# Performance work log

Hardware: AMD Instinct MI355X
Metric: run time of the kernel (lower is better)

Reference implementation:

```python
import jax, jax.numpy as jnp
import numpy as np

N_NODES = 100000
N_EDGES = 3200000
N_F = 128
HIDDEN = 128
N_PRED = 8
K_HOPS = 3
N_GRAPHS = 64


def setup_inputs() -> dict:
    key = jax.random.key(0)
    k1, k2, k3, k4, k5, k6, k7, k8 = jax.random.split(key, 8)
    x = jax.random.normal(k1, (N_NODES, N_F), dtype=jnp.float32)
    edge_index = jax.random.randint(k2, (2, N_EDGES), 0, N_NODES, dtype=jnp.int64)
    edge_attr = jax.random.uniform(k3, (N_EDGES,), dtype=jnp.float32)
    batch = jnp.sort(jax.random.randint(k4, (N_NODES,), 0, N_GRAPHS, dtype=jnp.int64))
    # SGConv internal Linear: in=n_f, out=hidden (applied after K propagations)
    s1 = 1.0 / np.sqrt(N_F)
    W_conv = jax.random.uniform(k5, (HIDDEN, N_F), dtype=jnp.float32, minval=-s1, maxval=s1)
    b_conv = jax.random.uniform(k6, (HIDDEN,), dtype=jnp.float32, minval=-s1, maxval=s1)
    s2 = 1.0 / np.sqrt(HIDDEN)
    W_lin = jax.random.uniform(k7, (N_PRED, HIDDEN), dtype=jnp.float32, minval=-s2, maxval=s2)
    b_lin = jax.random.uniform(k8, (N_PRED,), dtype=jnp.float32, minval=-s2, maxval=s2)
    return {"x": x, "edge_index": edge_index, "edge_attr": edge_attr, "batch": batch,
            "W_conv": W_conv, "b_conv": b_conv, "W_lin": W_lin, "b_lin": b_lin}


def _gcn_norm(edge_index, edge_weight, num_nodes):
    # Add self-loops with weight 1 (PyG gcn_norm default), then symmetric normalize.
    loop = jnp.arange(num_nodes, dtype=edge_index.dtype)
    row = jnp.concatenate([edge_index[0], loop])
    col = jnp.concatenate([edge_index[1], loop])
    w = jnp.concatenate([edge_weight, jnp.ones((num_nodes,), dtype=edge_weight.dtype)])
    deg = jax.ops.segment_sum(w, col, num_segments=num_nodes)
    dinv = jnp.where(deg > 0, jax.lax.rsqrt(jnp.where(deg > 0, deg, 1.0)), 0.0)
    norm = dinv[row] * w * dinv[col]
    return row, col, norm


def reference(x, edge_index, edge_attr, batch, W_conv, b_conv, W_lin, b_lin):
    N = x.shape[0]
    row, col, norm = _gcn_norm(edge_index, edge_attr, N)
    h = x
    for _ in range(K_HOPS):  # K repeated gather-scale-scatter propagations
        h = jax.ops.segment_sum(norm[:, None] * h[row], col, num_segments=N)
    h = h @ W_conv.T + b_conv  # SGConv linear: [N, hidden]
    # global_mean_pool by batch id
    sums = jax.ops.segment_sum(h, batch, num_segments=N_GRAPHS)
    cnt = jax.ops.segment_sum(jnp.ones((N,), dtype=h.dtype), batch, num_segments=N_GRAPHS)
    pooled = sums / jnp.maximum(cnt, 1.0)[:, None]
    # dropout(p=0.5) is identity in eval mode
    return pooled @ W_lin.T + b_lin
```

## Files before the change

kernel.cpp:

```cpp
#include <hip/hip_runtime.h>

#define NN 100000
#define NE 3200000
#define NF 128
#define NH 128
#define NP 8
#define NG 64

#define CS 16000
#define NC 7
#define NW 64
#define ES (NE / NW)

#define PT 64
#define GP 1024

#define SCAN_B 1024
#define SCAN_NBLK 98

__device__ __forceinline__ unsigned short f2bf(float f) {
    unsigned u = __float_as_uint(f);
    return (unsigned short)((u + 0x7fffu + ((u >> 16) & 1u)) >> 16);
}
__device__ __forceinline__ float bf2f(unsigned short b) {
    return __uint_as_float((unsigned)b << 16);
}

__global__ void k_init(float* __restrict__ cnt, float* __restrict__ psum) {
    int i = blockIdx.x * blockDim.x + threadIdx.x;
    if (i < NG) cnt[i] = 0.0f;
    if (i < NG * NH) psum[i] = 0.0f;
}

__global__ __launch_bounds__(256) void k_hist(const int* __restrict__ row,
                                              unsigned* __restrict__ H) {
    __shared__ unsigned hist[CS];
    int w = blockIdx.x % NW, c = blockIdx.x / NW;
    int rbase = c * CS;
    int nb = (rbase + CS <= NN) ? CS : (NN - rbase);
    for (int i = threadIdx.x; i < nb; i += 256) hist[i] = 0u;
    __syncthreads();
    const int4* r4 = (const int4*)(row + (size_t)w * ES);
    for (int i = threadIdx.x; i < ES / 8; i += 256) {
        int4 a = r4[2 * i], b = r4[2 * i + 1];
        int rs[8] = {a.x, a.y, a.z, a.w, b.x, b.y, b.z, b.w};
#pragma unroll
        for (int j = 0; j < 8; ++j) {
            unsigned rr = (unsigned)(rs[j] - rbase);
            if (rr < (unsigned)nb) atomicAdd(&hist[rr], 1u);
        }
    }
    __syncthreads();
    for (int i = threadIdx.x; i < nb; i += 256) H[(size_t)w * NN + rbase + i] = hist[i];
}

__global__ __launch_bounds__(256) void k_deg_hist(const int* __restrict__ col,
                                                  const float* __restrict__ wt,
                                                  float* __restrict__ Hd) {
    __shared__ float dh[CS];
    int w = blockIdx.x % NW, c = blockIdx.x / NW;
    int rbase = c * CS;
    int nb = (rbase + CS <= NN) ? CS : (NN - rbase);
    for (int i = threadIdx.x; i < nb; i += 256) dh[i] = 0.0f;
    __syncthreads();
    const int4*   c4 = (const int4*)(col + (size_t)w * ES);
    const float4* w4 = (const float4*)(wt + (size_t)w * ES);
    for (int i = threadIdx.x; i < ES / 8; i += 256) {
        int4 a = c4[2 * i], b = c4[2 * i + 1];
        float4 wa = w4[2 * i], wb = w4[2 * i + 1];
        int cc[8] = {a.x, a.y, a.z, a.w, b.x, b.y, b.z, b.w};
        float ww[8] = {wa.x, wa.y, wa.z, wa.w, wb.x, wb.y, wb.z, wb.w};
#pragma unroll
        for (int j = 0; j < 8; ++j) {
            unsigned rr = (unsigned)(cc[j] - rbase);
            if (rr < (unsigned)nb) atomicAdd(&dh[rr], ww[j]);
        }
    }
    __syncthreads();
    for (int i = threadIdx.x; i < nb; i += 256) Hd[(size_t)w * NN + rbase + i] = dh[i];
}

__global__ void k_cnt(const int* __restrict__ batch, float* __restrict__ cnt) {
    __shared__ float c[NG];
    int t = threadIdx.x;
    if (t < NG) c[t] = 0.0f;
    __syncthreads();
    int i = blockIdx.x * blockDim.x + t;
    if (i < NN) atomicAdd(&c[batch[i]], 1.0f);
    __syncthreads();
    if (t < NG && c[t] != 0.0f) atomicAdd(&cnt[t], c[t]);
}

__global__ void k_reduce(const unsigned* __restrict__ H, const float* __restrict__ Hd,
                         int* __restrict__ rcnt, float* __restrict__ dinv) {
    int r = blockIdx.x * blockDim.x + threadIdx.x;
    if (r >= NN) return;
    unsigned s = 0;
    float d = 1.0f;
#pragma unroll
    for (int w = 0; w < NW; ++w) {
        s += H[(size_t)w * NN + r];
        d += Hd[(size_t)w * NN + r];
    }
    rcnt[r] = (int)s;
    dinv[r] = rsqrtf(d);
}

__global__ __launch_bounds__(SCAN_B) void k_scan1(const int* __restrict__ rcnt,
                                                  int* __restrict__ px,
                                                  int* __restrict__ bsum) {
    __shared__ int s[SCAN_B];
    int t = threadIdx.x;
    int i = blockIdx.x * SCAN_B + t;
    int v = (i < NN) ? rcnt[i] : 0;
    s[t] = v;
    __syncthreads();
    for (int off = 1; off < SCAN_B; off <<= 1) {
        int x = (t >= off) ? s[t - off] : 0;
        __syncthreads();
        s[t] += x;
        __syncthreads();
    }
    px[i] = s[t] - v;
    if (t == SCAN_B - 1) bsum[blockIdx.x] = s[t];
}

__global__ void k_scan2(const int* __restrict__ bsum, int* __restrict__ bofs) {
    if (threadIdx.x == 0) {
        int acc = 0;
        for (int b = 0; b < SCAN_NBLK; ++b) { bofs[b] = acc; acc += bsum[b]; }
    }
}

__global__ void k_scan3(const int* __restrict__ px, const int* __restrict__ bofs,
                        int* __restrict__ rowptr) {
    int i = blockIdx.x * blockDim.x + threadIdx.x;
    if (i > NN) return;
    rowptr[i] = px[i] + bofs[i >> 10];
}

__global__ void k_base(const int* __restrict__ rowptr, unsigned* __restrict__ H) {
    int r = blockIdx.x * blockDim.x + threadIdx.x;
    if (r >= NN) return;
    unsigned acc = (unsigned)rowptr[r];
#pragma unroll
    for (int w = 0; w < NW; ++w) {
        unsigned v = H[(size_t)w * NN + r];
        H[(size_t)w * NN + r] = acc;
        acc += v;
    }
}

__global__ __launch_bounds__(256) void k_sort(const int* __restrict__ row,
                                              const int* __restrict__ col,
                                              const float* __restrict__ wt,
                                              const unsigned* __restrict__ B,
                                              const float* __restrict__ dinv,
                                              float2* __restrict__ pack) {
    __shared__ unsigned basel[CS];
    int w = blockIdx.x % NW, c = blockIdx.x / NW;
    int rbase = c * CS;
    int nb = (rbase + CS <= NN) ? CS : (NN - rbase);
    for (int i = threadIdx.x; i < nb; i += 256)
        basel[i] = B[(size_t)w * NN + rbase + i];
    __syncthreads();
    const int4*   r4 = (const int4*)(row + (size_t)w * ES);
    const int4*   c4 = (const int4*)(col + (size_t)w * ES);
    const float4* w4 = (const float4*)(wt + (size_t)w * ES);
    for (int i = threadIdx.x; i < ES / 8; i += 256) {
        int4 ra = r4[2 * i], rb = r4[2 * i + 1];
        int4 ca = c4[2 * i], cb = c4[2 * i + 1];
        float4 wa = w4[2 * i], wb = w4[2 * i + 1];
        int rs[8] = {ra.x, ra.y, ra.z, ra.w, rb.x, rb.y, rb.z, rb.w};
        int cs[8] = {ca.x, ca.y, ca.z, ca.w, cb.x, cb.y, cb.z, cb.w};
        float ww[8] = {wa.x, wa.y, wa.z, wa.w, wb.x, wb.y, wb.z, wb.w};
#pragma unroll
        for (int j = 0; j < 8; ++j) {
            unsigned rr = (unsigned)(rs[j] - rbase);
            if (rr < (unsigned)nb) {
                unsigned pos = atomicAdd(&basel[rr], 1u);
                pack[pos] = make_float2(__int_as_float(cs[j]),
                                        dinv[rs[j]] * ww[j] * dinv[cs[j]]);
            }
        }
    }
}

__global__ void k_q1_gather(const int* __restrict__ rowptr, const float2* __restrict__ pack,
                            const int* __restrict__ batch, const float* __restrict__ dinv,
                            unsigned short* __restrict__ Q) {
    int wid = (blockIdx.x * blockDim.x + threadIdx.x) >> 6;
    int lane = threadIdx.x & 63;
    if (wid >= NN) return;
    int es = lane >> 3;
    int gg = lane & 7;
    int beg = rowptr[wid], end = rowptr[wid + 1];
    float d = dinv[wid];
    int bself = batch[wid];
    float dd = d * d;
    float acc[8];
#pragma unroll
    for (int i = 0; i < 8; ++i)
        acc[i] = (es == 0 && bself == gg * 8 + i) ? dd : 0.0f;

    if (beg < end) {
        int last = end - 1;
        int idx0 = beg + es; if (idx0 > last) idx0 = last;
        float2 pe = pack[idx0];
        for (int e = beg; e < end; e += 8) {
            int nidx = e + 8 + es; if (nidx > last) nidx = last;
            float2 pnext = pack[nidx];
            int   cc = __float_as_int(pe.x);
            float w  = (e + es <= last) ? pe.y : 0.0f;
            int b = batch[cc];
#pragma unroll
            for (int i = 0; i < 8; ++i) acc[i] += (b == gg * 8 + i) ? w : 0.0f;
            pe = pnext;
        }
    }
#pragma unroll
    for (int m = 8; m <= 32; m <<= 1)
#pragma unroll
        for (int i = 0; i < 8; ++i) acc[i] += __shfl_xor(acc[i], m, 64);
    if (es == 0) {
        uint4 o;
        o.x = (unsigned)f2bf(acc[0]) | ((unsigned)f2bf(acc[1]) << 16);
        o.y = (unsigned)f2bf(acc[2]) | ((unsigned)f2bf(acc[3]) << 16);
        o.z = (unsigned)f2bf(acc[4]) | ((unsigned)f2bf(acc[5]) << 16);
        o.w = (unsigned)f2bf(acc[6]) | ((unsigned)f2bf(acc[7]) << 16);
        ((uint4*)Q)[(size_t)wid * 8 + gg] = o;
    }
}

__global__ void k_hop_gather(const int* __restrict__ rowptr, const float2* __restrict__ pack,
                             const float* __restrict__ dinv,
                             const unsigned short* __restrict__ Qin,
                             unsigned short* __restrict__ Qout) {
    int wid = (blockIdx.x * blockDim.x + threadIdx.x) >> 6;
    int lane = threadIdx.x & 63;
    if (wid >= NN) return;
    int es = lane >> 3;
    int gg = lane & 7;
    int beg = rowptr[wid], end = rowptr[wid + 1];
    float d = dinv[wid];
    const uint4* Q4 = (const uint4*)Qin;

    float acc[8];
    if (es == 0) {
        uint4 qs = Q4[(size_t)wid * 8 + gg];
        float dd = d * d;
        acc[0] = dd * __uint_as_float(qs.x << 16);
        acc[1] = dd * __uint_as_float(qs.x & 0xffff0000u);
        acc[2] = dd * __uint_as_float(qs.y << 16);
        acc[3] = dd * __uint_as_float(qs.y & 0xffff0000u);
        acc[4] = dd * __uint_as_float(qs.z << 16);
        acc[5] = dd * __uint_as_float(qs.z & 0xffff0000u);
        acc[6] = dd * __uint_as_float(qs.w << 16);
        acc[7] = dd * __uint_as_float(qs.w & 0xffff0000u);
    } else {
#pragma unroll
        for (int i = 0; i < 8; ++i) acc[i] = 0.0f;
    }

    if (beg < end) {
        int last = end - 1;
        int idx0 = beg + es; if (idx0 > last) idx0 = last;
        float2 pe = pack[idx0];
        for (int e = beg; e < end; e += 8) {
            int nidx = e + 8 + es; if (nidx > last) nidx = last;
            float2 pnext = pack[nidx];
            int   cc = __float_as_int(pe.x);
            float w  = (e + es <= last) ? pe.y : 0.0f;
            uint4 qv = Q4[(size_t)cc * 8 + gg];
            acc[0] += w * __uint_as_float(qv.x << 16);
            acc[1] += w * __uint_as_float(qv.x & 0xffff0000u);
            acc[2] += w * __uint_as_float(qv.y << 16);
            acc[3] += w * __uint_as_float(qv.y & 0xffff0000u);
            acc[4] += w * __uint_as_float(qv.z << 16);
            acc[5] += w * __uint_as_float(qv.z & 0xffff0000u);
            acc[6] += w * __uint_as_float(qv.w << 16);
            acc[7] += w * __uint_as_float(qv.w & 0xffff0000u);
            pe = pnext;
        }
    }
#pragma unroll
    for (int m = 8; m <= 32; m <<= 1)
#pragma unroll
        for (int i = 0; i < 8; ++i) acc[i] += __shfl_xor(acc[i], m, 64);
    if (es == 0) {
        uint4 o;
        o.x = (unsigned)f2bf(acc[0]) | ((unsigned)f2bf(acc[1]) << 16);
        o.y = (unsigned)f2bf(acc[2]) | ((unsigned)f2bf(acc[3]) << 16);
        o.z = (unsigned)f2bf(acc[4]) | ((unsigned)f2bf(acc[5]) << 16);
        o.w = (unsigned)f2bf(acc[6]) | ((unsigned)f2bf(acc[7]) << 16);
        ((uint4*)Qout)[(size_t)wid * 8 + gg] = o;
    }
}

__global__ __launch_bounds__(256) void k_pool(const unsigned short* __restrict__ Q,
                                              const float* __restrict__ x,
                                              float* __restrict__ partial) {
    __shared__ unsigned short qsh[PT * NG];
    __shared__ float xs[PT * NF];
    int t = threadIdx.x;
    int f4 = (t & 31) << 2;
    int g0 = (t >> 5) << 3;
    float4 acc[8];
#pragma unroll
    for (int i = 0; i < 8; ++i) acc[i] = make_float4(0.f, 0.f, 0.f, 0.f);

    const int NT = (NN + PT - 1) / PT;
    for (int tile = blockIdx.x; tile < NT; tile += GP) {
        int n0 = tile * PT;
        int nt = min(PT, NN - n0);
        const uint4*  Q4 = (const uint4*)(Q + (size_t)n0 * NG);
        const float4* X4 = (const float4*)(x + (size_t)n0 * NF);
        uint4*  qs4 = (uint4*)qsh;
        float4* xs4 = (float4*)xs;
        for (int i = t; i < nt * (NG / 8); i += 256) qs4[i] = Q4[i];
        for (int i = t; i < nt * (NF / 4); i += 256) xs4[i] = X4[i];
        __syncthreads();
        for (int n = 0; n < nt; ++n) {
            float4 xv = *(const float4*)&xs[n * NF + f4];
            uint4 qu = *(const uint4*)&qsh[n * NG + g0];
            float qv[8];
            qv[0] = __uint_as_float(qu.x << 16);
            qv[1] = __uint_as_float(qu.x & 0xffff0000u);
            qv[2] = __uint_as_float(qu.y << 16);
            qv[3] = __uint_as_float(qu.y & 0xffff0000u);
            qv[4] = __uint_as_float(qu.z << 16);
            qv[5] = __uint_as_float(qu.z & 0xffff0000u);
            qv[6] = __uint_as_float(qu.w << 16);
            qv[7] = __uint_as_float(qu.w & 0xffff0000u);
#pragma unroll
            for (int i = 0; i < 8; ++i) {
                acc[i].x += qv[i] * xv.x;
                acc[i].y += qv[i] * xv.y;
                acc[i].z += qv[i] * xv.z;
                acc[i].w += qv[i] * xv.w;
            }
        }
        __syncthreads();
    }
    float* pb = partial + (size_t)blockIdx.x * (NG * NF);
#pragma unroll
    for (int i = 0; i < 8; ++i)
        *(float4*)&pb[(g0 + i) * NF + f4] = acc[i];
}

__global__ void k_red(const float* __restrict__ partial, float* __restrict__ psum) {
    int gid = blockIdx.x * blockDim.x + threadIdx.x;
    int idx = gid & (NG * NF - 1);
    int j = gid >> 13;
    float acc = 0.0f;
    for (int b = j; b < GP; b += 8)
        acc += partial[(size_t)b * (NG * NF) + idx];
    atomicAdd(&psum[idx], acc);
}

__global__ void k_final(const float* __restrict__ psum, const float* __restrict__ cnt,
                        const float* __restrict__ Wc, const float* __restrict__ bc,
                        const float* __restrict__ Wl, const float* __restrict__ bl,
                        float* __restrict__ out) {
    __shared__ float M[NP * NH];
    __shared__ float bias[NP];
    int t = threadIdx.x;
    for (int idx = t; idx < NP * NH; idx += 256) {
        int p = idx >> 7, f = idx & 127;
        float s = 0.0f;
        for (int h = 0; h < NH; ++h) s += Wl[p * NH + h] * Wc[h * NF + f];
        M[idx] = s;
    }
    if (t < NP) {
        float s = bl[t];
        for (int h = 0; h < NH; ++h) s += Wl[t * NH + h] * bc[h];
        bias[t] = s;
    }
    __syncthreads();
    for (int idx = t; idx < NG * NP; idx += 256) {
        int g = idx >> 3, p = idx & 7;
        float inv = 1.0f / fmaxf(cnt[g], 1.0f);
        float s = 0.0f;
        for (int f = 0; f < NF; ++f) s += psum[g * NF + f] * M[p * NH + f];
        out[idx] = s * inv + bias[p];
    }
}

extern "C" void kernel_launch(void* const* d_in, const int* in_sizes, int n_in,
                              void* d_out, int out_size, void* d_ws, size_t ws_size,
                              hipStream_t stream) {
    const float* x     = (const float*)d_in[0];
    const int*   ei    = (const int*)d_in[1];
    const float* ea    = (const float*)d_in[2];
    const int*   batch = (const int*)d_in[3];
    const float* Wc    = (const float*)d_in[4];
    const float* bc    = (const float*)d_in[5];
    const float* Wl    = (const float*)d_in[6];
    const float* bl    = (const float*)d_in[7];
    const int* row = ei;
    const int* col = ei + NE;
    float* out = (float*)d_out;

    float* ws     = (float*)d_ws;
    float*  dinv   = ws;
    int*    rowptr = (int*)(dinv + NN);
    float*  cnt    = (float*)(rowptr + NN + 4);
    float*  psum   = cnt + NG;
    float2* pack   = (float2*)(psum + NG * NH);
    unsigned* H    = (unsigned*)(pack + NE);
    float*    Hd   = (float*)(H + (size_t)NW * NN);
    unsigned short* Qa = (unsigned short*)H;
    unsigned short* Qb = Qa + (size_t)NN * NG;
    float* partial = (float*)Qb;
    int* rcnt = (int*)pack;
    int* px   = rcnt + SCAN_NBLK * SCAN_B;
    int* bsum = px + SCAN_NBLK * SCAN_B;
    int* bofs = bsum + SCAN_NBLK;

    const int B = 256;
    int gN  = (NN + B - 1) / B;
    int gCW = NC * NW;
    int gW  = (int)(((long long)NN * 64 + B - 1) / B);

    k_init<<<(NG * NH + B - 1) / B, B, 0, stream>>>(cnt, psum);
    k_hist<<<gCW, B, 0, stream>>>(row, H);
    k_deg_hist<<<gCW, B, 0, stream>>>(col, ea, Hd);
    k_cnt<<<gN, B, 0, stream>>>(batch, cnt);
    k_reduce<<<gN, B, 0, stream>>>(H, Hd, rcnt, dinv);

    k_scan1<<<SCAN_NBLK, SCAN_B, 0, stream>>>(rcnt, px, bsum);
    k_scan2<<<1, 64, 0, stream>>>(bsum, bofs);
    k_scan3<<<(NN + 1 + SCAN_B - 1) / SCAN_B, SCAN_B, 0, stream>>>(px, bofs, rowptr);
    k_base<<<gN, B, 0, stream>>>(rowptr, H);
    k_sort<<<gCW, B, 0, stream>>>(row, col, ea, H, dinv, pack);

    k_q1_gather<<<gW, B, 0, stream>>>(rowptr, pack, batch, dinv, Qa);
    k_hop_gather<<<gW, B, 0, stream>>>(rowptr, pack, dinv, Qa, Qb);
    k_hop_gather<<<gW, B, 0, stream>>>(rowptr, pack, dinv, Qb, Qa);

    k_pool<<<GP, B, 0, stream>>>(Qa, x, partial);
    k_red<<<256, B, 0, stream>>>(partial, psum);
    k_final<<<1, B, 0, stream>>>(psum, cnt, Wc, bc, Wl, bl, out);
}
```

Before: 615.1 us.

## Split Q into four graph-column planes and propagate each plane separately

Stores the 64-column bf16 Q matrix as four planes of 16 graph columns each, and runs the two remaining hop propagations once per plane. Each plane is small enough to stay cache-resident during its random gathers. The hop kernel now uses 32 edge slots by 2 halves per wave, and edge pack loads and Q stores are non-temporal. The first gather also unrolls four edges per iteration. In exchange, the edge list and rowptr are read four times as often and more kernels are launched.

```diff
diff --git a/kernel.cpp b/kernel.cpp
--- a/kernel.cpp
+++ b/kernel.cpp
@@ -17,6 +17,8 @@
 
 #define SCAN_B 1024
 #define SCAN_NBLK 98
+
+#define PLANE ((size_t)NN * 16)
 
 __device__ __forceinline__ unsigned short f2bf(float f) {
     unsigned u = __float_as_uint(f);
@@ -184,6 +186,14 @@
             }
         }
     }
+}
+
+__device__ __forceinline__ void pk_nt(const float2* __restrict__ pack, int idx,
+                                      int& cc, float& w) {
+    unsigned long long pu =
+        __builtin_nontemporal_load((const unsigned long long*)pack + idx);
+    cc = (int)(unsigned)pu;
+    w = __uint_as_float((unsigned)(pu >> 32));
 }
 
 __global__ void k_q1_gather(const int* __restrict__ rowptr, const float2* __restrict__ pack,
@@ -205,17 +215,29 @@
 
     if (beg < end) {
         int last = end - 1;
-        int idx0 = beg + es; if (idx0 > last) idx0 = last;
-        float2 pe = pack[idx0];
-        for (int e = beg; e < end; e += 8) {
-            int nidx = e + 8 + es; if (nidx > last) nidx = last;
-            float2 pnext = pack[nidx];
-            int   cc = __float_as_int(pe.x);
-            float w  = (e + es <= last) ? pe.y : 0.0f;
-            int b = batch[cc];
-#pragma unroll
-            for (int i = 0; i < 8; ++i) acc[i] += (b == gg * 8 + i) ? w : 0.0f;
-            pe = pnext;
+        for (int e = beg; e < end; e += 32) {
+            int i0 = e + es, i1 = e + 8 + es, i2 = e + 16 + es, i3 = e + 24 + es;
+            int c0, c1, c2, c3; float w0, w1, w2, w3;
+            pk_nt(pack, min(i0, last), c0, w0);
+            pk_nt(pack, min(i1, last), c1, w1);
+            pk_nt(pack, min(i2, last), c2, w2);
+            pk_nt(pack, min(i3, last), c3, w3);
+            if (i0 > last) w0 = 0.0f;
+            if (i1 > last) w1 = 0.0f;
+            if (i2 > last) w2 = 0.0f;
+            if (i3 > last) w3 = 0.0f;
+            int b0 = batch[c0];
+            int b1 = batch[c1];
+            int b2 = batch[c2];
+            int b3 = batch[c3];
+#pragma unroll
+            for (int i = 0; i < 8; ++i) {
+                int g = gg * 8 + i;
+                acc[i] += (b0 == g) ? w0 : 0.0f;
+                acc[i] += (b1 == g) ? w1 : 0.0f;
+                acc[i] += (b2 == g) ? w2 : 0.0f;
+                acc[i] += (b3 == g) ? w3 : 0.0f;
+            }
         }
     }
 #pragma unroll
@@ -228,26 +250,27 @@
         o.y = (unsigned)f2bf(acc[2]) | ((unsigned)f2bf(acc[3]) << 16);
         o.z = (unsigned)f2bf(acc[4]) | ((unsigned)f2bf(acc[5]) << 16);
         o.w = (unsigned)f2bf(acc[6]) | ((unsigned)f2bf(acc[7]) << 16);
-        ((uint4*)Q)[(size_t)wid * 8 + gg] = o;
-    }
-}
-
-__global__ void k_hop_gather(const int* __restrict__ rowptr, const float2* __restrict__ pack,
-                             const float* __restrict__ dinv,
-                             const unsigned short* __restrict__ Qin,
-                             unsigned short* __restrict__ Qout) {
+        ((uint4*)Q)[(size_t)(gg >> 1) * ((size_t)NN * 2) + (size_t)wid * 2 + (gg & 1)] = o;
+    }
+}
+
+__global__ __launch_bounds__(256) void k_hop16(const int* __restrict__ rowptr,
+                                               const float2* __restrict__ pack,
+                                               const float* __restrict__ dinv,
+                                               const unsigned short* __restrict__ Qin,
+                                               unsigned short* __restrict__ Qout) {
     int wid = (blockIdx.x * blockDim.x + threadIdx.x) >> 6;
     int lane = threadIdx.x & 63;
     if (wid >= NN) return;
-    int es = lane >> 3;
-    int gg = lane & 7;
+    int es = lane >> 1;
+    int hf = lane & 1;
     int beg = rowptr[wid], end = rowptr[wid + 1];
-    float d = dinv[wid];
     const uint4* Q4 = (const uint4*)Qin;
 
     float acc[8];
     if (es == 0) {
-        uint4 qs = Q4[(size_t)wid * 8 + gg];
+        uint4 qs = Q4[(size_t)wid * 2 + hf];
+        float d = dinv[wid];
         float dd = d * d;
         acc[0] = dd * __uint_as_float(qs.x << 16);
         acc[1] = dd * __uint_as_float(qs.x & 0xffff0000u);
@@ -264,14 +287,13 @@
 
     if (beg < end) {
         int last = end - 1;
-        int idx0 = beg + es; if (idx0 > last) idx0 = last;
-        float2 pe = pack[idx0];
-        for (int e = beg; e < end; e += 8) {
-            int nidx = e + 8 + es; if (nidx > last) nidx = last;
-            float2 pnext = pack[nidx];
-            int   cc = __float_as_int(pe.x);
-            float w  = (e + es <= last) ? pe.y : 0.0f;
-            uint4 qv = Q4[(size_t)cc * 8 + gg];
+        int cc; float w;
+        pk_nt(pack, min(beg + es, last), cc, w);
+        for (int e = beg; e < end; e += 32) {
+            int cn; float wn;
+            pk_nt(pack, min(e + 32 + es, last), cn, wn);
+            if (e + es > last) w = 0.0f;
+            uint4 qv = Q4[(size_t)cc * 2 + hf];
             acc[0] += w * __uint_as_float(qv.x << 16);
             acc[1] += w * __uint_as_float(qv.x & 0xffff0000u);
             acc[2] += w * __uint_as_float(qv.y << 16);
@@ -280,20 +302,24 @@
             acc[5] += w * __uint_as_float(qv.z & 0xffff0000u);
             acc[6] += w * __uint_as_float(qv.w << 16);
             acc[7] += w * __uint_as_float(qv.w & 0xffff0000u);
-            pe = pnext;
-        }
-    }
-#pragma unroll
-    for (int m = 8; m <= 32; m <<= 1)
+            cc = cn; w = wn;
+        }
+    }
+#pragma unroll
+    for (int m = 2; m <= 32; m <<= 1)
 #pragma unroll
         for (int i = 0; i < 8; ++i) acc[i] += __shfl_xor(acc[i], m, 64);
     if (es == 0) {
-        uint4 o;
-        o.x = (unsigned)f2bf(acc[0]) | ((unsigned)f2bf(acc[1]) << 16);
-        o.y = (unsigned)f2bf(acc[2]) | ((unsigned)f2bf(acc[3]) << 16);
-        o.z = (unsigned)f2bf(acc[4]) | ((unsigned)f2bf(acc[5]) << 16);
-        o.w = (unsigned)f2bf(acc[6]) | ((unsigned)f2bf(acc[7]) << 16);
-        ((uint4*)Qout)[(size_t)wid * 8 + gg] = o;
+        unsigned long long lo =
+            (unsigned long long)((unsigned)f2bf(acc[0]) | ((unsigned)f2bf(acc[1]) << 16)) |
+            ((unsigned long long)((unsigned)f2bf(acc[2]) | ((unsigned)f2bf(acc[3]) << 16)) << 32);
+        unsigned long long hi =
+            (unsigned long long)((unsigned)f2bf(acc[4]) | ((unsigned)f2bf(acc[5]) << 16)) |
+            ((unsigned long long)((unsigned)f2bf(acc[6]) | ((unsigned)f2bf(acc[7]) << 16)) << 32);
+        unsigned long long* dst =
+            (unsigned long long*)Qout + ((size_t)wid * 2 + hf) * 2;
+        __builtin_nontemporal_store(lo, dst);
+        __builtin_nontemporal_store(hi, dst + 1);
     }
 }
 
@@ -309,15 +335,19 @@
 #pragma unroll
     for (int i = 0; i < 8; ++i) acc[i] = make_float4(0.f, 0.f, 0.f, 0.f);
 
+    const uint4* Qb4 = (const uint4*)Q;
     const int NT = (NN + PT - 1) / PT;
     for (int tile = blockIdx.x; tile < NT; tile += GP) {
         int n0 = tile * PT;
         int nt = min(PT, NN - n0);
-        const uint4*  Q4 = (const uint4*)(Q + (size_t)n0 * NG);
         const float4* X4 = (const float4*)(x + (size_t)n0 * NF);
         uint4*  qs4 = (uint4*)qsh;
         float4* xs4 = (float4*)xs;
-        for (int i = t; i < nt * (NG / 8); i += 256) qs4[i] = Q4[i];
+        for (int i = t; i < nt * 8; i += 256) {
+            int rrow = i >> 3, j = i & 7;
+            qs4[rrow * 8 + j] = Qb4[(size_t)(j >> 1) * ((size_t)NN * 2)
+                                    + (size_t)(n0 + rrow) * 2 + (j & 1)];
+        }
         for (int i = t; i < nt * (NF / 4); i += 256) xs4[i] = X4[i];
         __syncthreads();
         for (int n = 0; n < nt; ++n) {
@@ -435,8 +465,13 @@
     k_sort<<<gCW, B, 0, stream>>>(row, col, ea, H, dinv, pack);
 
     k_q1_gather<<<gW, B, 0, stream>>>(rowptr, pack, batch, dinv, Qa);
-    k_hop_gather<<<gW, B, 0, stream>>>(rowptr, pack, dinv, Qa, Qb);
-    k_hop_gather<<<gW, B, 0, stream>>>(rowptr, pack, dinv, Qb, Qa);
+
+    for (int p = 0; p < 4; ++p) {
+        unsigned short* Qap = Qa + (size_t)p * PLANE;
+        unsigned short* Qbp = Qb + (size_t)p * PLANE;
+        k_hop16<<<gW, B, 0, stream>>>(rowptr, pack, dinv, Qap, Qbp);
+        k_hop16<<<gW, B, 0, stream>>>(rowptr, pack, dinv, Qbp, Qap);
+    }
 
     k_pool<<<GP, B, 0, stream>>>(Qa, x, partial);
     k_red<<<256, B, 0, stream>>>(partial, psum);
```

After: 827.6 us. 1.35x slower.
